# Optimization experiments

Measured on AMD Instinct MI355X. Metric: run time of the kernel, lower is better.

## Reference

```python
import jax, jax.numpy as jnp
import numpy as np

GENE_DIM = 1024
REDUCED_DIM = 128
RADIUS = 100.0
THRESH = 0.01
ALPHA = 2.0


def setup_inputs() -> dict:
    key = jax.random.key(0)
    ks = jax.random.split(key, 12)
    B, K, D, R = 4096, 32, GENE_DIM, REDUCED_DIM
    s = 1.0 / np.sqrt(D)
    return {
        "target_cell": jax.random.normal(ks[0], (B, D), jnp.float32),
        "neighbors": jax.random.normal(ks[1], (B, K, D), jnp.float32),
        "distances": jax.random.uniform(ks[2], (B, K), jnp.float32) * RADIUS,
        "beta": jnp.asarray(0.5, jnp.float32),
        "ln_scale": jnp.ones((D,), jnp.float32),
        "ln_bias": jnp.zeros((D,), jnp.float32),
        "w_self": jax.random.normal(ks[3], (D, D), jnp.float32) * s,
        "b_self": jnp.zeros((D,), jnp.float32),
        "w_nb": jax.random.normal(ks[4], (D, D), jnp.float32) * s,
        "b_nb": jnp.zeros((D,), jnp.float32),
        "w_red": jax.random.normal(ks[5], (R, D), jnp.float32) * s,
        "b_red": jnp.zeros((R,), jnp.float32),
    }


def _layer_norm(x, scale, bias, eps=1e-5):
    mu = jnp.mean(x, axis=-1, keepdims=True)
    var = jnp.mean(jnp.square(x - mu), axis=-1, keepdims=True)
    return (x - mu) * jax.lax.rsqrt(var + eps) * scale + bias


def reference(target_cell, neighbors, distances, beta, ln_scale, ln_bias,
              w_self, b_self, w_nb, b_nb, w_red, b_red):
    tc = _layer_norm(target_cell, ln_scale, ln_bias)          # [B, D]
    nb = _layer_norm(neighbors, ln_scale, ln_bias)            # [B, K, D]
    self_scores = tc @ w_self.T + b_self                      # [B, D]
    nb_scores = jnp.einsum("bkd,ed->bke", nb, w_nb) + b_nb    # [B, K, D]
    dist_w = jnp.exp(-ALPHA * distances / (RADIUS + 1e-8))    # [B, K]
    weighted_nb = nb_scores * dist_w[:, :, None]
    combined = jnp.concatenate([self_scores[:, None, :], weighted_nb], axis=1)  # [B, K+1, D]
    cw = jax.nn.softmax(combined, axis=1)
    self_w = cw[:, 0, :]                                      # [B, D]
    nb_w = cw[:, 1:, :]                                       # [B, K, D]
    self_w = jnp.where(jnp.abs(self_w) >= THRESH, self_w, 0.0)
    nb_w = jnp.where(jnp.abs(nb_w) >= THRESH, nb_w, 0.0)
    context = beta * (self_w * tc) + (1.0 - beta) * jnp.sum(nb_w * nb, axis=1)
    reduced = jax.nn.leaky_relu(context @ w_red.T + b_red, negative_slope=0.01)
    return (reduced, self_w, nb_w)
```

## Files before the change

### kernel.cpp

```cpp
#include <hip/hip_runtime.h>
#include <stdint.h>

constexpr int Bc = 4096;
constexpr int Kc = 32;
constexpr int Dc = 1024;
constexpr int Rc = 128;
constexpr int MNB = Bc * Kc;

typedef __attribute__((ext_vector_type(8))) short short8;
typedef __attribute__((ext_vector_type(4))) float floatx4;

__device__ __forceinline__ unsigned short f2bf(float x) {
  union { float f; uint32_t u; } v; v.f = x;
  return (unsigned short)((v.u + 0x7fffu + ((v.u >> 16) & 1u)) >> 16);
}
__device__ __forceinline__ float bf2f(unsigned short b) {
  union { float f; uint32_t u; } v; v.u = ((uint32_t)b) << 16;
  return v.f;
}

__device__ __forceinline__ void async_copy16(const void* g, void* l) {
  __builtin_amdgcn_global_load_lds(
      (const __attribute__((address_space(1))) void*)g,
      (__attribute__((address_space(3))) void*)l, 16, 0, 0);
}

__global__ __launch_bounds__(256) void ln_kernel(
    const float* __restrict__ target, const float* __restrict__ neighbors,
    const float* __restrict__ scale, const float* __restrict__ bias,
    unsigned short* __restrict__ tc_bf, unsigned short* __restrict__ nb_bf) {
  int row = blockIdx.x;
  const float* src;
  unsigned short* dst;
  if (row < Bc) {
    src = target + (size_t)row * Dc;
    dst = tc_bf + (size_t)row * Dc;
  } else {
    size_t r2 = (size_t)(row - Bc);
    src = neighbors + r2 * Dc;
    dst = nb_bf + r2 * Dc;
  }
  int t = threadIdx.x;
  float4 x = ((const float4*)src)[t];
  float s = x.x + x.y + x.z + x.w;
  float ss = x.x * x.x + x.y * x.y + x.z * x.z + x.w * x.w;
#pragma unroll
  for (int m = 32; m >= 1; m >>= 1) {
    s += __shfl_xor(s, m, 64);
    ss += __shfl_xor(ss, m, 64);
  }
  __shared__ float red[8];
  int wave = t >> 6, lane = t & 63;
  if (lane == 0) { red[wave] = s; red[wave + 4] = ss; }
  __syncthreads();
  s = red[0] + red[1] + red[2] + red[3];
  ss = red[4] + red[5] + red[6] + red[7];
  float mu = s * (1.0f / Dc);
  float var = ss * (1.0f / Dc) - mu * mu;
  float rstd = rsqrtf(var + 1e-5f);
  float4 sc = ((const float4*)scale)[t];
  float4 bi = ((const float4*)bias)[t];
  ushort4 o;
  o.x = f2bf((x.x - mu) * rstd * sc.x + bi.x);
  o.y = f2bf((x.y - mu) * rstd * sc.y + bi.y);
  o.z = f2bf((x.z - mu) * rstd * sc.z + bi.z);
  o.w = f2bf((x.w - mu) * rstd * sc.w + bi.w);
  ((ushort4*)dst)[t] = o;
}

__global__ __launch_bounds__(256) void conv_kernel(
    const float* __restrict__ src, unsigned short* __restrict__ dst, int n4) {
  int i = blockIdx.x * 256 + threadIdx.x;
  if (i < n4) {
    float4 x = ((const float4*)src)[i];
    ushort4 o;
    o.x = f2bf(x.x); o.y = f2bf(x.y); o.z = f2bf(x.z); o.w = f2bf(x.w);
    ((ushort4*)dst)[i] = o;
  }
}

template <int EPI>
__global__ __launch_bounds__(256) void gemm_bf16(
    const unsigned short* __restrict__ A, const unsigned short* __restrict__ Bm,
    const float* __restrict__ bias, float* __restrict__ C,
    int M, int N, int Kd, int NN, int NMdiv8) {
  __shared__ short Alds[128 * 64];
  __shared__ short Blds[128 * 64];

  int g = blockIdx.x;
  int xcd = g & 7;
  int t = g >> 3;
  int bn = t % NN;
  int bm = xcd * NMdiv8 + t / NN;

  int tid = threadIdx.x;
  int wave = tid >> 6;
  int lane = tid & 63;
  int wm = (wave >> 1) * 64;
  int wn = (wave & 1) * 64;

  floatx4 acc[4][4];
#pragma unroll
  for (int mi = 0; mi < 4; ++mi)
#pragma unroll
    for (int ni = 0; ni < 4; ++ni) {
      floatx4 z = {0.f, 0.f, 0.f, 0.f};
      acc[mi][ni] = z;
    }

  int srow = lane >> 3;
  int scol = (lane & 7) * 8;
  size_t lda = (size_t)Kd;

  for (int k0 = 0; k0 < Kd; k0 += 64) {
#pragma unroll
    for (int i = 0; i < 4; ++i) {
      int grp = wave * 4 + i;
      int rA = grp * 8 + srow;
      const unsigned short* gA = A + ((size_t)(bm * 128 + rA)) * lda + k0 + scol;
      const unsigned short* gB = Bm + ((size_t)(bn * 128 + rA)) * lda + k0 + scol;
      async_copy16(gA, &Alds[grp * 512]);
      async_copy16(gB, &Blds[grp * 512]);
    }
    __syncthreads();
#pragma unroll
    for (int ks = 0; ks < 2; ++ks) {
      short8 af[4], bf[4];
#pragma unroll
      for (int mi = 0; mi < 4; ++mi)
        af[mi] = *(const short8*)&Alds[(wm + mi * 16 + (lane & 15)) * 64 +
                                       ks * 32 + (lane >> 4) * 8];
#pragma unroll
      for (int ni = 0; ni < 4; ++ni)
        bf[ni] = *(const short8*)&Blds[(wn + ni * 16 + (lane & 15)) * 64 +
                                       ks * 32 + (lane >> 4) * 8];
#pragma unroll
      for (int mi = 0; mi < 4; ++mi)
#pragma unroll
        for (int ni = 0; ni < 4; ++ni)
          acc[mi][ni] = __builtin_amdgcn_mfma_f32_16x16x32_bf16(
              af[mi], bf[ni], acc[mi][ni], 0, 0, 0);
    }
    __syncthreads();
  }

  int quad = lane >> 4;
  int col15 = lane & 15;
#pragma unroll
  for (int mi = 0; mi < 4; ++mi) {
#pragma unroll
    for (int ni = 0; ni < 4; ++ni) {
      int n_g = bn * 128 + wn + ni * 16 + col15;
      float bv = bias[n_g];
#pragma unroll
      for (int r = 0; r < 4; ++r) {
        int m_g = bm * 128 + wm + mi * 16 + quad * 4 + r;
        float v = acc[mi][ni][r] + bv;
        if (EPI == 1) v = (v > 0.f) ? v : 0.01f * v;
        C[(size_t)m_g * N + n_g] = v;
      }
    }
  }
}

__global__ __launch_bounds__(256) void gemm_nb_fused(
    const unsigned short* __restrict__ A, const unsigned short* __restrict__ Bm,
    const float* __restrict__ bias, const float* __restrict__ distances,
    const float* __restrict__ beta_p, const unsigned short* __restrict__ tc_bf,
    float* __restrict__ selfsc, float* __restrict__ nbw,
    unsigned short* __restrict__ ctx_bf) {
  __shared__ short Alds[128 * 64];
  __shared__ short Blds[128 * 64];
  __shared__ float dw_lds[128];

  constexpr int NN = 8;
  constexpr int NMdiv8 = 128;
  int g = blockIdx.x;
  int xcd = g & 7;
  int t = g >> 3;
  int bn = t % NN;
  int bm = xcd * NMdiv8 + t / NN;
  int b0 = bm * 4;

  int tid = threadIdx.x;
  int wave = tid >> 6;
  int lane = tid & 63;
  int wm = (wave >> 1) * 64;
  int wn = (wave & 1) * 64;

  if (tid < 128) {
    int b_loc = tid >> 5, k = tid & 31;
    dw_lds[tid] = __expf((float)(-2.0 / 100.00000001) *
                         distances[(size_t)(b0 + b_loc) * Kc + k]);
  }

  floatx4 acc[4][4];
#pragma unroll
  for (int mi = 0; mi < 4; ++mi)
#pragma unroll
    for (int ni = 0; ni < 4; ++ni) {
      floatx4 z = {0.f, 0.f, 0.f, 0.f};
      acc[mi][ni] = z;
    }

  int srow = lane >> 3;
  int scol = (lane & 7) * 8;
  size_t lda = (size_t)Dc;

  for (int k0 = 0; k0 < Dc; k0 += 64) {
#pragma unroll
    for (int i = 0; i < 4; ++i) {
      int grp = wave * 4 + i;
      int rA = grp * 8 + srow;
      const unsigned short* gA = A + ((size_t)(bm * 128 + rA)) * lda + k0 + scol;
      const unsigned short* gB = Bm + ((size_t)(bn * 128 + rA)) * lda + k0 + scol;
      async_copy16(gA, &Alds[grp * 512]);
      async_copy16(gB, &Blds[grp * 512]);
    }
    __syncthreads();
#pragma unroll
    for (int ks = 0; ks < 2; ++ks) {
      short8 af[4], bf[4];
#pragma unroll
      for (int mi = 0; mi < 4; ++mi)
        af[mi] = *(const short8*)&Alds[(wm + mi * 16 + (lane & 15)) * 64 +
                                       ks * 32 + (lane >> 4) * 8];
#pragma unroll
      for (int ni = 0; ni < 4; ++ni)
        bf[ni] = *(const short8*)&Blds[(wn + ni * 16 + (lane & 15)) * 64 +
                                       ks * 32 + (lane >> 4) * 8];
#pragma unroll
      for (int mi = 0; mi < 4; ++mi)
#pragma unroll
        for (int ni = 0; ni < 4; ++ni)
          acc[mi][ni] = __builtin_amdgcn_mfma_f32_16x16x32_bf16(
              af[mi], bf[ni], acc[mi][ni], 0, 0, 0);
    }
    __syncthreads();
  }

  int quad = lane >> 4;
  int col15 = lane & 15;
  float beta = beta_p[0];
  float omb = 1.0f - beta;

#pragma unroll
  for (int ni = 0; ni < 4; ++ni) {
    int n_g = bn * 128 + wn + ni * 16 + col15;
    float bv = bias[n_g];
#pragma unroll
    for (int bh = 0; bh < 2; ++bh) {
      int b_loc = (wave >> 1) * 2 + bh;
      int b = b0 + b_loc;
      size_t bd = (size_t)b * Dc + n_g;

      float l[8];
      float mx = -1e30f;
#pragma unroll
      for (int mo = 0; mo < 2; ++mo)
#pragma unroll
        for (int r = 0; r < 4; ++r) {
          int k = mo * 16 + quad * 4 + r;
          float v = (acc[bh * 2 + mo][ni][r] + bv) * dw_lds[b_loc * 32 + k];
          l[mo * 4 + r] = v;
          mx = fmaxf(mx, v);
        }
      mx = fmaxf(mx, __shfl_xor(mx, 16, 64));
      mx = fmaxf(mx, __shfl_xor(mx, 32, 64));
      float l0 = selfsc[bd];
      mx = fmaxf(mx, l0);

      float sum = 0.f;
#pragma unroll
      for (int i = 0; i < 8; ++i) {
        l[i] = __expf(l[i] - mx);
        sum += l[i];
      }
      sum += __shfl_xor(sum, 16, 64);
      sum += __shfl_xor(sum, 32, 64);
      float e0 = __expf(l0 - mx);
      float inv = 1.0f / (sum + e0);

      float w0 = e0 * inv;
      if (w0 < 0.01f) w0 = 0.f;

      float ctxn = 0.f;
#pragma unroll
      for (int mo = 0; mo < 2; ++mo)
#pragma unroll
        for (int r = 0; r < 4; ++r) {
          int k = mo * 16 + quad * 4 + r;
          float w = l[mo * 4 + r] * inv;
          if (w < 0.01f) w = 0.f;
          size_t idx = ((size_t)(b * Kc + k)) * Dc + n_g;
          nbw[idx] = w;
          ctxn += w * bf2f(A[idx]);
        }
      ctxn += __shfl_xor(ctxn, 16, 64);
      ctxn += __shfl_xor(ctxn, 32, 64);

      if (quad == 0) {
        selfsc[bd] = w0;
        float ctx = beta * w0 * bf2f(tc_bf[bd]) + omb * ctxn;
        ctx_bf[bd] = f2bf(ctx);
      }
    }
  }
}

extern "C" void kernel_launch(void* const* d_in, const int* in_sizes, int n_in,
                              void* d_out, int out_size, void* d_ws,
                              size_t ws_size, hipStream_t stream) {
  const float* target    = (const float*)d_in[0];
  const float* neighbors = (const float*)d_in[1];
  const float* distances = (const float*)d_in[2];
  const float* beta      = (const float*)d_in[3];
  const float* ln_scale  = (const float*)d_in[4];
  const float* ln_bias   = (const float*)d_in[5];
  const float* w_self    = (const float*)d_in[6];
  const float* b_self    = (const float*)d_in[7];
  const float* w_nb      = (const float*)d_in[8];
  const float* b_nb      = (const float*)d_in[9];
  const float* w_red     = (const float*)d_in[10];
  const float* b_red     = (const float*)d_in[11];

  float* out = (float*)d_out;
  float* reduced = out;
  float* selfw   = out + (size_t)Bc * Rc;
  float* nbw     = selfw + (size_t)Bc * Dc;

  char* ws = (char*)d_ws;
  unsigned short* nb_bf   = (unsigned short*)ws;
  unsigned short* tc_bf   = (unsigned short*)(ws + 268435456);
  unsigned short* ctx_bf  = (unsigned short*)(ws + 276824064);
  unsigned short* wself_bf = (unsigned short*)(ws + 285212672);
  unsigned short* wnb_bf   = (unsigned short*)(ws + 287309824);
  unsigned short* wred_bf  = (unsigned short*)(ws + 289406976);

  ln_kernel<<<Bc + MNB, 256, 0, stream>>>(target, neighbors, ln_scale, ln_bias,
                                          tc_bf, nb_bf);
  conv_kernel<<<1024, 256, 0, stream>>>(w_self, wself_bf, 262144);
  conv_kernel<<<1024, 256, 0, stream>>>(w_nb, wnb_bf, 262144);
  conv_kernel<<<128, 256, 0, stream>>>(w_red, wred_bf, 32768);
  gemm_bf16<0><<<256, 256, 0, stream>>>(tc_bf, wself_bf, b_self, selfw,
                                        Bc, Dc, Dc, 8, 4);
  gemm_nb_fused<<<8192, 256, 0, stream>>>(nb_bf, wnb_bf, b_nb, distances, beta,
                                          tc_bf, selfw, nbw, ctx_bf);
  gemm_bf16<1><<<32, 256, 0, stream>>>(ctx_bf, wred_bf, b_red, reduced,
                                       Bc, Rc, Dc, 1, 4);
}
```

Baseline: 1.582 ms.

## Double-buffer GEMM LDS tiles and XOR-swizzle LDS layout to cut bank conflicts

```diff
diff --git a/kernel.cpp b/kernel.cpp
--- a/kernel.cpp
+++ b/kernel.cpp
@@ -23,6 +23,21 @@
   __builtin_amdgcn_global_load_lds(
       (const __attribute__((address_space(1))) void*)g,
       (__attribute__((address_space(3))) void*)l, 16, 0, 0);
+}
+
+__device__ __forceinline__ void stage_tile(
+    const unsigned short* __restrict__ A, const unsigned short* __restrict__ Bm,
+    short* Al, short* Bl, int bmBase, int bnBase, size_t lda, int k0,
+    int wave, int srow, int scol) {
+#pragma unroll
+  for (int i = 0; i < 4; ++i) {
+    int grp = wave * 4 + i;
+    int rA = grp * 8 + srow;
+    const unsigned short* gA = A + ((size_t)(bmBase + rA)) * lda + k0 + scol;
+    const unsigned short* gB = Bm + ((size_t)(bnBase + rA)) * lda + k0 + scol;
+    async_copy16(gA, &Al[grp * 512]);
+    async_copy16(gB, &Bl[grp * 512]);
+  }
 }
 
 __global__ __launch_bounds__(256) void ln_kernel(
@@ -84,8 +99,8 @@
     const unsigned short* __restrict__ A, const unsigned short* __restrict__ Bm,
     const float* __restrict__ bias, float* __restrict__ C,
     int M, int N, int Kd, int NN, int NMdiv8) {
-  __shared__ short Alds[128 * 64];
-  __shared__ short Blds[128 * 64];
+  __shared__ short Alds[2][128 * 64];
+  __shared__ short Blds[2][128 * 64];
 
   int g = blockIdx.x;
   int xcd = g & 7;
@@ -98,6 +113,9 @@
   int lane = tid & 63;
   int wm = (wave >> 1) * 64;
   int wn = (wave & 1) * 64;
+  int quad = lane >> 4;
+  int l15 = lane & 15;
+  int x7 = lane & 7;
 
   floatx4 acc[4][4];
 #pragma unroll
@@ -109,42 +127,41 @@
     }
 
   int srow = lane >> 3;
-  int scol = (lane & 7) * 8;
+  int scol = ((lane & 7) ^ srow) * 8;
   size_t lda = (size_t)Kd;
-
-  for (int k0 = 0; k0 < Kd; k0 += 64) {
-#pragma unroll
-    for (int i = 0; i < 4; ++i) {
-      int grp = wave * 4 + i;
-      int rA = grp * 8 + srow;
-      const unsigned short* gA = A + ((size_t)(bm * 128 + rA)) * lda + k0 + scol;
-      const unsigned short* gB = Bm + ((size_t)(bn * 128 + rA)) * lda + k0 + scol;
-      async_copy16(gA, &Alds[grp * 512]);
-      async_copy16(gB, &Blds[grp * 512]);
-    }
-    __syncthreads();
+  int NT = Kd >> 6;
+
+  stage_tile(A, Bm, Alds[0], Blds[0], bm * 128, bn * 128, lda, 0, wave, srow, scol);
+  __syncthreads();
+
+  for (int tk = 0; tk < NT; ++tk) {
+    int cur = tk & 1;
+    if (tk + 1 < NT)
+      stage_tile(A, Bm, Alds[cur ^ 1], Blds[cur ^ 1], bm * 128, bn * 128, lda,
+                 (tk + 1) * 64, wave, srow, scol);
+    const short* Ab = Alds[cur];
+    const short* Bb = Blds[cur];
 #pragma unroll
     for (int ks = 0; ks < 2; ++ks) {
-      short8 af[4], bf[4];
+      short8 af[4], bfr[4];
 #pragma unroll
       for (int mi = 0; mi < 4; ++mi)
-        af[mi] = *(const short8*)&Alds[(wm + mi * 16 + (lane & 15)) * 64 +
-                                       ks * 32 + (lane >> 4) * 8];
+        af[mi] = *(const short8*)&Ab[(wm + mi * 16 + l15) * 64 +
+                                     (((ks * 4 + quad) ^ x7) << 3)];
 #pragma unroll
       for (int ni = 0; ni < 4; ++ni)
-        bf[ni] = *(const short8*)&Blds[(wn + ni * 16 + (lane & 15)) * 64 +
-                                       ks * 32 + (lane >> 4) * 8];
+        bfr[ni] = *(const short8*)&Bb[(wn + ni * 16 + l15) * 64 +
+                                      (((ks * 4 + quad) ^ x7) << 3)];
 #pragma unroll
       for (int mi = 0; mi < 4; ++mi)
 #pragma unroll
         for (int ni = 0; ni < 4; ++ni)
           acc[mi][ni] = __builtin_amdgcn_mfma_f32_16x16x32_bf16(
-              af[mi], bf[ni], acc[mi][ni], 0, 0, 0);
+              af[mi], bfr[ni], acc[mi][ni], 0, 0, 0);
     }
     __syncthreads();
   }
 
-  int quad = lane >> 4;
   int col15 = lane & 15;
 #pragma unroll
   for (int mi = 0; mi < 4; ++mi) {
@@ -169,8 +186,8 @@
     const float* __restrict__ beta_p, const unsigned short* __restrict__ tc_bf,
     float* __restrict__ selfsc, float* __restrict__ nbw,
     unsigned short* __restrict__ ctx_bf) {
-  __shared__ short Alds[128 * 64];
-  __shared__ short Blds[128 * 64];
+  __shared__ short Alds[2][128 * 64];
+  __shared__ short Blds[2][128 * 64];
   __shared__ float dw_lds[128];
 
   constexpr int NN = 8;
@@ -187,6 +204,9 @@
   int lane = tid & 63;
   int wm = (wave >> 1) * 64;
   int wn = (wave & 1) * 64;
+  int quad = lane >> 4;
+  int l15 = lane & 15;
+  int x7 = lane & 7;
 
   if (tid < 128) {
     int b_loc = tid >> 5, k = tid & 31;
@@ -204,42 +224,41 @@
     }
 
   int srow = lane >> 3;
-  int scol = (lane & 7) * 8;
+  int scol = ((lane & 7) ^ srow) * 8;
   size_t lda = (size_t)Dc;
-
-  for (int k0 = 0; k0 < Dc; k0 += 64) {
-#pragma unroll
-    for (int i = 0; i < 4; ++i) {
-      int grp = wave * 4 + i;
-      int rA = grp * 8 + srow;
-      const unsigned short* gA = A + ((size_t)(bm * 128 + rA)) * lda + k0 + scol;
-      const unsigned short* gB = Bm + ((size_t)(bn * 128 + rA)) * lda + k0 + scol;
-      async_copy16(gA, &Alds[grp * 512]);
-      async_copy16(gB, &Blds[grp * 512]);
-    }
-    __syncthreads();
+  constexpr int NT = Dc >> 6;
+
+  stage_tile(A, Bm, Alds[0], Blds[0], bm * 128, bn * 128, lda, 0, wave, srow, scol);
+  __syncthreads();
+
+  for (int tk = 0; tk < NT; ++tk) {
+    int cur = tk & 1;
+    if (tk + 1 < NT)
+      stage_tile(A, Bm, Alds[cur ^ 1], Blds[cur ^ 1], bm * 128, bn * 128, lda,
+                 (tk + 1) * 64, wave, srow, scol);
+    const short* Ab = Alds[cur];
+    const short* Bb = Blds[cur];
 #pragma unroll
     for (int ks = 0; ks < 2; ++ks) {
-      short8 af[4], bf[4];
+      short8 af[4], bfr[4];
 #pragma unroll
       for (int mi = 0; mi < 4; ++mi)
-        af[mi] = *(const short8*)&Alds[(wm + mi * 16 + (lane & 15)) * 64 +
-                                       ks * 32 + (lane >> 4) * 8];
+        af[mi] = *(const short8*)&Ab[(wm + mi * 16 + l15) * 64 +
+                                     (((ks * 4 + quad) ^ x7) << 3)];
 #pragma unroll
       for (int ni = 0; ni < 4; ++ni)
-        bf[ni] = *(const short8*)&Blds[(wn + ni * 16 + (lane & 15)) * 64 +
-                                       ks * 32 + (lane >> 4) * 8];
+        bfr[ni] = *(const short8*)&Bb[(wn + ni * 16 + l15) * 64 +
+                                      (((ks * 4 + quad) ^ x7) << 3)];
 #pragma unroll
       for (int mi = 0; mi < 4; ++mi)
 #pragma unroll
         for (int ni = 0; ni < 4; ++ni)
           acc[mi][ni] = __builtin_amdgcn_mfma_f32_16x16x32_bf16(
-              af[mi], bf[ni], acc[mi][ni], 0, 0, 0);
+              af[mi], bfr[ni], acc[mi][ni], 0, 0, 0);
     }
     __syncthreads();
   }
 
-  int quad = lane >> 4;
   int col15 = lane & 15;
   float beta = beta_p[0];
   float omb = 1.0f - beta;
```

Result: faster. 1.543 ms (-2.5%).
